# Kernel optimization log

Measured on AMD Instinct MI355X. Metric: run time of the kernel, lower is better.

The kernel has to match this reference:

```python
import jax, jax.numpy as jnp
import numpy as np

N_NODES = 50000


def gcn_layer(x, W, b, src, dst, n_nodes):
    # PyG GCNConv(normalize=True): add self-loops, deg^-1/2 sym norm,
    # x' = D^-1/2 (A+I) D^-1/2 (x W) + b, aggregation at dst (col).
    h = x @ W  # [N, out]
    ones = jnp.ones(src.shape[0], dtype=h.dtype)
    deg = jax.ops.segment_sum(ones, dst, num_segments=n_nodes) + 1.0  # +1 self-loop
    dinv = jax.lax.rsqrt(deg)  # [N]
    norm = dinv[src] * dinv[dst]  # per-edge coefficient
    msg = h[src] * norm[:, None]  # [E, out] gather
    agg = jax.ops.segment_sum(msg, dst, num_segments=n_nodes)  # scatter-add
    agg = agg + h * (dinv * dinv)[:, None]  # self-loop term (norm = dinv_i^2)
    return agg + b


def setup_inputs() -> dict:
    key = jax.random.key(0)
    k1, k2, k3, k4, k5 = jax.random.split(key, 5)
    x = jax.random.normal(k1, (N_NODES, 96), dtype=jnp.float32)
    edge_index = jax.random.randint(k2, (2, 800000), 0, N_NODES, dtype=jnp.int64)
    # Glorot-ish weights, zero bias (PyG default init style)
    W1 = jax.random.normal(k3, (96, 96), dtype=jnp.float32) * (1.0 / np.sqrt(96))
    b1 = jnp.zeros((96,), dtype=jnp.float32)
    W2 = jax.random.normal(k4, (96, 64), dtype=jnp.float32) * (1.0 / np.sqrt(96))
    b2 = jnp.zeros((64,), dtype=jnp.float32)
    return {"x": x, "edge_index": edge_index, "W1": W1, "b1": b1, "W2": W2, "b2": b2}


def reference(x, edge_index, W1, b1, W2, b2):
    src, dst = edge_index[0], edge_index[1]
    n = x.shape[0]
    h = gcn_layer(x, W1, b1, src, dst, n)
    out = gcn_layer(h, W2, b2, src, dst, n)
    return out
```

## Files before the change

### kernel.cpp

```cpp
#include <hip/hip_runtime.h>

#define N_NODES 50000
#define N_EDGES 800000
#define NBLKA 200
#define EPB (N_EDGES / NBLKA)
#define NBUCK 196
#define MSCAN (256 * NBLKA)
#define GEMMBLKS ((N_NODES + 63) / 64)

typedef unsigned int uint;
typedef unsigned short ushort;

__device__ __forceinline__ uint bf16pack(float a, float b) {
    uint ua = __float_as_uint(a); ua = (ua + 0x7FFFu + ((ua >> 16) & 1u)) >> 16;
    uint ub = __float_as_uint(b); ub = (ub + 0x7FFFu + ((ub >> 16) & 1u)) >> 16;
    return ua | (ub << 16);
}
#define BF_LO(U) __uint_as_float((U) << 16)
#define BF_HI(U) __uint_as_float((U) & 0xFFFF0000u)

__global__ void histA_kernel(const int* __restrict__ dst, int* __restrict__ hist) {
    __shared__ int h[256];
    h[threadIdx.x] = 0;
    __syncthreads();
    int base = blockIdx.x * EPB;
    for (int i = base + threadIdx.x; i < base + EPB; i += 256)
        atomicAdd(&h[dst[i] >> 8], 1);
    __syncthreads();
    hist[threadIdx.x * NBLKA + blockIdx.x] = h[threadIdx.x];
}

__global__ void scan1_kernel(const int* __restrict__ in, int* __restrict__ out,
                             int* __restrict__ bsum, int n) {
    __shared__ int s[256];
    int i = blockIdx.x * 256 + threadIdx.x;
    int v = (i < n) ? in[i] : 0;
    s[threadIdx.x] = v;
    __syncthreads();
    for (int d = 1; d < 256; d <<= 1) {
        int t = (threadIdx.x >= d) ? s[threadIdx.x - d] : 0;
        __syncthreads();
        s[threadIdx.x] += t;
        __syncthreads();
    }
    if (i < n) out[i] = s[threadIdx.x] - v;
    if (threadIdx.x == 255) bsum[blockIdx.x] = s[255];
}

__global__ void scan2_wfuse_kernel(int* __restrict__ bsum, int* __restrict__ boff, int nb,
                                   const float* __restrict__ W1, const float* __restrict__ W2,
                                   const float* __restrict__ b1, float* __restrict__ W12,
                                   float* __restrict__ bw) {
    if (blockIdx.x == 0) {
        __shared__ int s[256];
        int t = threadIdx.x;
        int v = (t < nb) ? bsum[t] : 0;
        s[t] = v;
        __syncthreads();
        for (int d = 1; d < 256; d <<= 1) {
            int x = (t >= d) ? s[t - d] : 0;
            __syncthreads();
            s[t] += x;
            __syncthreads();
        }
        if (t < nb) boff[t] = s[t] - v;
        if (t == nb - 1) boff[nb] = s[t];
    } else {
        int idx = (blockIdx.x - 1) * 256 + threadIdx.x;
        if (idx < 96 * 64) {
            int k = idx >> 6, nn = idx & 63;
            float s = 0.0f;
#pragma unroll
            for (int j = 0; j < 96; ++j) s = fmaf(W1[k * 96 + j], W2[j * 64 + nn], s);
            W12[idx] = s;
        } else if (idx < 96 * 64 + 64) {
            int nn = idx - 96 * 64;
            float s = 0.0f;
#pragma unroll
            for (int j = 0; j < 96; ++j) s = fmaf(b1[j], W2[j * 64 + nn], s);
            bw[nn] = s;
        }
    }
}

#define FMA4(ACC, SCL, WV)                                                     \
    ACC.x = fmaf(SCL, WV.x, ACC.x);                                            \
    ACC.y = fmaf(SCL, WV.y, ACC.y);                                            \
    ACC.z = fmaf(SCL, WV.z, ACC.z);                                            \
    ACC.w = fmaf(SCL, WV.w, ACC.w);

__global__ __launch_bounds__(256)
void scatter_gemm_kernel(const int* __restrict__ src, const int* __restrict__ dst,
                         const int* __restrict__ scanned, const int* __restrict__ boff,
                         int2* __restrict__ ebuf,
                         const float* __restrict__ A, const float* __restrict__ W,
                         ushort* __restrict__ y16, int M) {
    __shared__ float smem[96 * 64 + 64 * 100];
    int tid = threadIdx.x;

    if (blockIdx.x < NBLKA) {
        int* off = (int*)smem;
        int gi = tid * NBLKA + blockIdx.x;
        off[tid] = scanned[gi] + boff[gi >> 8];
        __syncthreads();
        int base = blockIdx.x * EPB;
        for (int i = base + tid; i < base + EPB; i += 256) {
            int s = src[i];
            int d = dst[i];
            int p = atomicAdd(&off[d >> 8], 1);
            ebuf[p] = make_int2(s, d);
        }
        return;
    }

    int bid = blockIdx.x - NBLKA;
    float* sW = smem;
    float* sA = smem + 96 * 64;
    {
        const float4* W4 = (const float4*)W;
        float4* sW4 = (float4*)sW;
        for (int i = tid; i < 96 * 16; i += 256) sW4[i] = W4[i];
    }
    long row0 = (long)bid * 64;
    {
        const float4* A4 = (const float4*)A;
        long base4 = row0 * 24;
        long lim = (long)M * 24 - 1;
        for (int f = tid; f < 64 * 24; f += 256) {
            long g = base4 + f;
            if (g > lim) g = lim;
            float4 v = A4[g];
            int r = f / 24, kc = f - r * 24;
            *(float4*)(sA + r * 100 + kc * 4) = v;
        }
    }
    __syncthreads();

    int tx = tid & 15;
    int ty = tid >> 4;
    float4 acc0 = {0, 0, 0, 0};
    float4 acc1 = {0, 0, 0, 0};
    float4 acc2 = {0, 0, 0, 0};
    float4 acc3 = {0, 0, 0, 0};
    const float* pa = sA + ty * 4 * 100;
    const float* pw = sW + tx * 4;

#pragma unroll 1
    for (int k = 0; k < 96; k += 4) {
        float4 a0 = *(const float4*)(pa + 0 * 100 + k);
        float4 a1 = *(const float4*)(pa + 1 * 100 + k);
        float4 a2 = *(const float4*)(pa + 2 * 100 + k);
        float4 a3 = *(const float4*)(pa + 3 * 100 + k);
        float4 w0 = *(const float4*)(pw + (k + 0) * 64);
        float4 w1 = *(const float4*)(pw + (k + 1) * 64);
        float4 w2 = *(const float4*)(pw + (k + 2) * 64);
        float4 w3 = *(const float4*)(pw + (k + 3) * 64);
        FMA4(acc0, a0.x, w0) FMA4(acc0, a0.y, w1) FMA4(acc0, a0.z, w2) FMA4(acc0, a0.w, w3)
        FMA4(acc1, a1.x, w0) FMA4(acc1, a1.y, w1) FMA4(acc1, a1.z, w2) FMA4(acc1, a1.w, w3)
        FMA4(acc2, a2.x, w0) FMA4(acc2, a2.y, w1) FMA4(acc2, a2.z, w2) FMA4(acc2, a2.w, w3)
        FMA4(acc3, a3.x, w0) FMA4(acc3, a3.y, w1) FMA4(acc3, a3.z, w2) FMA4(acc3, a3.w, w3)
    }

    long r0 = row0 + ty * 4;
    uint2 p0 = {bf16pack(acc0.x, acc0.y), bf16pack(acc0.z, acc0.w)};
    uint2 p1 = {bf16pack(acc1.x, acc1.y), bf16pack(acc1.z, acc1.w)};
    uint2 p2 = {bf16pack(acc2.x, acc2.y), bf16pack(acc2.z, acc2.w)};
    uint2 p3 = {bf16pack(acc3.x, acc3.y), bf16pack(acc3.z, acc3.w)};
    if (r0 + 0 < M) *(uint2*)(y16 + (r0 + 0) * 64 + tx * 4) = p0;
    if (r0 + 1 < M) *(uint2*)(y16 + (r0 + 1) * 64 + tx * 4) = p1;
    if (r0 + 2 < M) *(uint2*)(y16 + (r0 + 2) * 64 + tx * 4) = p2;
    if (r0 + 3 < M) *(uint2*)(y16 + (r0 + 3) * 64 + tx * 4) = p3;
}

__global__ void bucket_kernel(const int2* __restrict__ ebuf, const int* __restrict__ scanned,
                              const int* __restrict__ boff, int* __restrict__ rowstart,
                              float* __restrict__ dinv, int* __restrict__ esrc) {
    __shared__ int cnt[256];
    __shared__ int cur[256];
    __shared__ int s[256];
    int k = blockIdx.x;
    int tid = threadIdx.x;
    int i0 = k * NBLKA, i1 = (k + 1) * NBLKA;
    int base = scanned[i0] + boff[i0 >> 8];
    int end  = (k == NBUCK - 1) ? N_EDGES : (scanned[i1] + boff[i1 >> 8]);
    cnt[tid] = 0;
    __syncthreads();
    for (int i = base + tid; i < end; i += 256)
        atomicAdd(&cnt[ebuf[i].y & 255], 1);
    __syncthreads();
    int v = cnt[tid];
    s[tid] = v;
    __syncthreads();
    for (int d = 1; d < 256; d <<= 1) {
        int t = (tid >= d) ? s[tid - d] : 0;
        __syncthreads();
        s[tid] += t;
        __syncthreads();
    }
    int excl = s[tid] - v;
    int node = (k << 8) + tid;
    cur[tid] = base + excl;
    if (node < N_NODES) {
        rowstart[node] = base + excl;
        dinv[node] = rsqrtf((float)v + 1.0f);
    }
    if (k == 0 && tid == 0) rowstart[N_NODES] = N_EDGES;
    __syncthreads();
    for (int i = base + tid; i < end; i += 256) {
        int2 e = ebuf[i];
        int p = atomicAdd(&cur[e.y & 255], 1);
        esrc[p] = e.x;
    }
}

#define DECFMA(A0, A1, A2, A3, A4, A5, A6, A7, C, V)                           \
    A0 = fmaf(BF_LO(V.x), C, A0); A1 = fmaf(BF_HI(V.x), C, A1);                \
    A2 = fmaf(BF_LO(V.y), C, A2); A3 = fmaf(BF_HI(V.y), C, A3);                \
    A4 = fmaf(BF_LO(V.z), C, A4); A5 = fmaf(BF_HI(V.z), C, A5);                \
    A6 = fmaf(BF_LO(V.w), C, A6); A7 = fmaf(BF_HI(V.w), C, A7);

template <bool FINAL>
__global__ __launch_bounds__(256)
void agg_kernel(const ushort* __restrict__ yin, const int* __restrict__ rowstart,
                const int* __restrict__ esrc, const float* __restrict__ dinv,
                const float* __restrict__ bw, const float* __restrict__ b2,
                ushort* __restrict__ zout, float* __restrict__ fout, int n) {
    int wid = (blockIdx.x * blockDim.x + threadIdx.x) >> 6;
    int lane = threadIdx.x & 63;
    if (wid >= n) return;
    int rs = rowstart[wid];
    int re = rowstart[wid + 1];
    float di = dinv[wid];
    int sub = lane >> 3;
    int q = lane & 7;
    const uint4* yrow = (const uint4*)yin;
    float P0 = 0, P1 = 0, P2 = 0, P3 = 0, P4 = 0, P5 = 0, P6 = 0, P7 = 0;
    float Q0 = 0, Q1 = 0, Q2 = 0, Q3 = 0, Q4 = 0, Q5 = 0, Q6 = 0, Q7 = 0;
    float sd = 0.0f;

    for (int base = rs; base < re; base += 64) {
        int idx = base + lane;
        bool ok = idx < re;
        int sj = ok ? esrc[idx] : 0;
        float dj = ok ? dinv[sj] : 0.0f;
        sd += dj;
        int nn = re - base;
        if (nn > 64) nn = 64;
#pragma unroll 1
        for (int it = 0; it * 32 < nn; ++it) {
            int e0 = it * 32 + sub;
            int s0 = __shfl(sj, e0);      float c0 = __shfl(dj, e0);
            int s1 = __shfl(sj, e0 + 8);  float c1 = __shfl(dj, e0 + 8);
            int s2 = __shfl(sj, e0 + 16); float c2 = __shfl(dj, e0 + 16);
            int s3 = __shfl(sj, e0 + 24); float c3 = __shfl(dj, e0 + 24);
            uint4 v0 = yrow[(long)s0 * 8 + q];
            uint4 v1 = yrow[(long)s1 * 8 + q];
            uint4 v2 = yrow[(long)s2 * 8 + q];
            uint4 v3 = yrow[(long)s3 * 8 + q];
            DECFMA(P0, P1, P2, P3, P4, P5, P6, P7, c0, v0)
            DECFMA(Q0, Q1, Q2, Q3, Q4, Q5, Q6, Q7, c1, v1)
            DECFMA(P0, P1, P2, P3, P4, P5, P6, P7, c2, v2)
            DECFMA(Q0, Q1, Q2, Q3, Q4, Q5, Q6, Q7, c3, v3)
        }
    }

    float t0 = P0 + Q0, t1 = P1 + Q1, t2 = P2 + Q2, t3 = P3 + Q3;
    float t4 = P4 + Q4, t5 = P5 + Q5, t6 = P6 + Q6, t7 = P7 + Q7;
    t0 += __shfl_xor(t0, 8); t0 += __shfl_xor(t0, 16); t0 += __shfl_xor(t0, 32);
    t1 += __shfl_xor(t1, 8); t1 += __shfl_xor(t1, 16); t1 += __shfl_xor(t1, 32);
    t2 += __shfl_xor(t2, 8); t2 += __shfl_xor(t2, 16); t2 += __shfl_xor(t2, 32);
    t3 += __shfl_xor(t3, 8); t3 += __shfl_xor(t3, 16); t3 += __shfl_xor(t3, 32);
    t4 += __shfl_xor(t4, 8); t4 += __shfl_xor(t4, 16); t4 += __shfl_xor(t4, 32);
    t5 += __shfl_xor(t5, 8); t5 += __shfl_xor(t5, 16); t5 += __shfl_xor(t5, 32);
    t6 += __shfl_xor(t6, 8); t6 += __shfl_xor(t6, 16); t6 += __shfl_xor(t6, 32);
    t7 += __shfl_xor(t7, 8); t7 += __shfl_xor(t7, 16); t7 += __shfl_xor(t7, 32);

    uint4 sv = yrow[(long)wid * 8 + q];
    float dii = di * di;
    float o0 = fmaf(t0, di, BF_LO(sv.x) * dii);
    float o1 = fmaf(t1, di, BF_HI(sv.x) * dii);
    float o2 = fmaf(t2, di, BF_LO(sv.y) * dii);
    float o3 = fmaf(t3, di, BF_HI(sv.y) * dii);
    float o4 = fmaf(t4, di, BF_LO(sv.z) * dii);
    float o5 = fmaf(t5, di, BF_HI(sv.z) * dii);
    float o6 = fmaf(t6, di, BF_LO(sv.w) * dii);
    float o7 = fmaf(t7, di, BF_HI(sv.w) * dii);

    if (FINAL) {
#pragma unroll
        for (int m = 1; m < 64; m <<= 1) sd += __shfl_xor(sd, m);
        float si = di * (di + sd);
        int fo = q * 8;
        float4 bwa = *(const float4*)(bw + fo);
        float4 bwb = *(const float4*)(bw + fo + 4);
        float4 b2a = *(const float4*)(b2 + fo);
        float4 b2b = *(const float4*)(b2 + fo + 4);
        o0 = fmaf(si, bwa.x, o0) + b2a.x;
        o1 = fmaf(si, bwa.y, o1) + b2a.y;
        o2 = fmaf(si, bwa.z, o2) + b2a.z;
        o3 = fmaf(si, bwa.w, o3) + b2a.w;
        o4 = fmaf(si, bwb.x, o4) + b2b.x;
        o5 = fmaf(si, bwb.y, o5) + b2b.y;
        o6 = fmaf(si, bwb.z, o6) + b2b.z;
        o7 = fmaf(si, bwb.w, o7) + b2b.w;
        if (sub == 0) {
            float4 wa = {o0, o1, o2, o3};
            float4 wb = {o4, o5, o6, o7};
            *(float4*)(fout + (long)wid * 64 + q * 8) = wa;
            *(float4*)(fout + (long)wid * 64 + q * 8 + 4) = wb;
        }
    } else {
        if (sub == 0) {
            uint4 pk;
            pk.x = bf16pack(o0, o1);
            pk.y = bf16pack(o2, o3);
            pk.z = bf16pack(o4, o5);
            pk.w = bf16pack(o6, o7);
            *(uint4*)(zout + (long)wid * 64 + q * 8) = pk;
        }
    }
}

extern "C" void kernel_launch(void* const* d_in, const int* in_sizes, int n_in,
                              void* d_out, int out_size, void* d_ws, size_t ws_size,
                              hipStream_t stream) {
    const float* x  = (const float*)d_in[0];
    const int*   ei = (const int*)d_in[1];
    const float* W1 = (const float*)d_in[2];
    const float* b1 = (const float*)d_in[3];
    const float* W2 = (const float*)d_in[4];
    const float* b2 = (const float*)d_in[5];
    float* out = (float*)d_out;

    const int* src = ei;
    const int* dst = ei + N_EDGES;

    char* ws = (char*)d_ws;
    float*  dinv     = (float*) (ws + 0);
    int*    rowstart = (int*)   (ws + 204800);
    int*    hist     = (int*)   (ws + 409600);
    int*    scanned  = (int*)   (ws + 614400);
    int*    bsum     = (int*)   (ws + 823296);
    int*    boff     = (int*)   (ws + 824320);
    float*  W12      = (float*) (ws + 825344);
    float*  bw       = (float*) (ws + 849920);
    int*    esrc     = (int*)   (ws + 850432);
    ushort* y16      = (ushort*)(ws + 4050432);
    int2*   ebuf     = (int2*)  (ws + 10450432);
    ushort* z16      = (ushort*)(ws + 10450432);

    histA_kernel<<<NBLKA, 256, 0, stream>>>(dst, hist);
    scan1_kernel<<<MSCAN / 256, 256, 0, stream>>>(hist, scanned, bsum, MSCAN);
    scan2_wfuse_kernel<<<26, 256, 0, stream>>>(bsum, boff, MSCAN / 256,
                                               W1, W2, b1, W12, bw);
    scatter_gemm_kernel<<<NBLKA + GEMMBLKS, 256, 0, stream>>>(
        src, dst, scanned, boff, ebuf, x, W12, y16, N_NODES);

    bucket_kernel<<<NBUCK, 256, 0, stream>>>(ebuf, scanned, boff, rowstart, dinv, esrc);

    int aggBlocks = (N_NODES + 3) / 4;
    agg_kernel<false><<<aggBlocks, 256, 0, stream>>>(y16, rowstart, esrc, dinv,
                                                     bw, b2, z16, out, N_NODES);
    agg_kernel<true><<<aggBlocks, 256, 0, stream>>>(z16, rowstart, esrc, dinv,
                                                    bw, b2, z16, out, N_NODES);
}
```

Baseline: 98.97 us.

## Assign 16 lanes per node in aggregation and pack edge indices into 16 bits

The aggregation kernels now give each node a 16-lane group instead of a full 64-lane wavefront, so four nodes share a wavefront. With an average in-degree around 16, most lanes in the old layout sat idle. The reductions shrink to fit the smaller group. Separately, the sort buffer packs the source index and the low 8 bits of the destination into one 32-bit word, and the CSR source array becomes 16-bit, which cuts the bytes moved in the bucket and aggregation passes. This only works while the node count stays below 65536, and each lane now issues fewer independent gathers in flight.

```diff
diff --git a/kernel.cpp b/kernel.cpp
--- a/kernel.cpp
+++ b/kernel.cpp
@@ -92,7 +92,7 @@
 __global__ __launch_bounds__(256)
 void scatter_gemm_kernel(const int* __restrict__ src, const int* __restrict__ dst,
                          const int* __restrict__ scanned, const int* __restrict__ boff,
-                         int2* __restrict__ ebuf,
+                         uint* __restrict__ ebuf,
                          const float* __restrict__ A, const float* __restrict__ W,
                          ushort* __restrict__ y16, int M) {
     __shared__ float smem[96 * 64 + 64 * 100];
@@ -108,7 +108,7 @@
             int s = src[i];
             int d = dst[i];
             int p = atomicAdd(&off[d >> 8], 1);
-            ebuf[p] = make_int2(s, d);
+            ebuf[p] = (uint)s | ((uint)(d & 255) << 16);
         }
         return;
     }
@@ -172,9 +172,9 @@
     if (r0 + 3 < M) *(uint2*)(y16 + (r0 + 3) * 64 + tx * 4) = p3;
 }
 
-__global__ void bucket_kernel(const int2* __restrict__ ebuf, const int* __restrict__ scanned,
+__global__ void bucket_kernel(const uint* __restrict__ ebuf, const int* __restrict__ scanned,
                               const int* __restrict__ boff, int* __restrict__ rowstart,
-                              float* __restrict__ dinv, int* __restrict__ esrc) {
+                              float* __restrict__ dinv, ushort* __restrict__ esrc) {
     __shared__ int cnt[256];
     __shared__ int cur[256];
     __shared__ int s[256];
@@ -186,7 +186,7 @@
     cnt[tid] = 0;
     __syncthreads();
     for (int i = base + tid; i < end; i += 256)
-        atomicAdd(&cnt[ebuf[i].y & 255], 1);
+        atomicAdd(&cnt[(ebuf[i] >> 16) & 255], 1);
     __syncthreads();
     int v = cnt[tid];
     s[tid] = v;
@@ -207,9 +207,9 @@
     if (k == 0 && tid == 0) rowstart[N_NODES] = N_EDGES;
     __syncthreads();
     for (int i = base + tid; i < end; i += 256) {
-        int2 e = ebuf[i];
-        int p = atomicAdd(&cur[e.y & 255], 1);
-        esrc[p] = e.x;
+        uint e = ebuf[i];
+        int p = atomicAdd(&cur[(e >> 16) & 255], 1);
+        esrc[p] = (ushort)(e & 0xFFFFu);
     }
 }
 
@@ -222,60 +222,50 @@
 template <bool FINAL>
 __global__ __launch_bounds__(256)
 void agg_kernel(const ushort* __restrict__ yin, const int* __restrict__ rowstart,
-                const int* __restrict__ esrc, const float* __restrict__ dinv,
+                const ushort* __restrict__ esrc, const float* __restrict__ dinv,
                 const float* __restrict__ bw, const float* __restrict__ b2,
                 ushort* __restrict__ zout, float* __restrict__ fout, int n) {
-    int wid = (blockIdx.x * blockDim.x + threadIdx.x) >> 6;
-    int lane = threadIdx.x & 63;
-    if (wid >= n) return;
-    int rs = rowstart[wid];
-    int re = rowstart[wid + 1];
-    float di = dinv[wid];
-    int sub = lane >> 3;
-    int q = lane & 7;
+    int gid = (blockIdx.x * blockDim.x + threadIdx.x) >> 4;
+    int gl = threadIdx.x & 15;
+    if (gid >= n) return;
+    int rs = rowstart[gid];
+    int re = rowstart[gid + 1];
+    float di = dinv[gid];
+    int sub = gl >> 3;
+    int q = gl & 7;
+    int wbase = (threadIdx.x & 63) & 48;
     const uint4* yrow = (const uint4*)yin;
     float P0 = 0, P1 = 0, P2 = 0, P3 = 0, P4 = 0, P5 = 0, P6 = 0, P7 = 0;
-    float Q0 = 0, Q1 = 0, Q2 = 0, Q3 = 0, Q4 = 0, Q5 = 0, Q6 = 0, Q7 = 0;
     float sd = 0.0f;
 
-    for (int base = rs; base < re; base += 64) {
-        int idx = base + lane;
+    for (int base = rs; base < re; base += 16) {
+        int idx = base + gl;
         bool ok = idx < re;
-        int sj = ok ? esrc[idx] : 0;
+        int sj = ok ? (int)esrc[idx] : 0;
         float dj = ok ? dinv[sj] : 0.0f;
         sd += dj;
         int nn = re - base;
-        if (nn > 64) nn = 64;
-#pragma unroll 1
-        for (int it = 0; it * 32 < nn; ++it) {
-            int e0 = it * 32 + sub;
-            int s0 = __shfl(sj, e0);      float c0 = __shfl(dj, e0);
-            int s1 = __shfl(sj, e0 + 8);  float c1 = __shfl(dj, e0 + 8);
-            int s2 = __shfl(sj, e0 + 16); float c2 = __shfl(dj, e0 + 16);
-            int s3 = __shfl(sj, e0 + 24); float c3 = __shfl(dj, e0 + 24);
+        if (nn > 16) nn = 16;
+        for (int it = 0; it * 2 < nn; ++it) {
+            int e = it * 2 + sub;
+            int sl = wbase + e;
+            int s0 = __shfl(sj, sl);
+            float c0 = __shfl(dj, sl);
             uint4 v0 = yrow[(long)s0 * 8 + q];
-            uint4 v1 = yrow[(long)s1 * 8 + q];
-            uint4 v2 = yrow[(long)s2 * 8 + q];
-            uint4 v3 = yrow[(long)s3 * 8 + q];
             DECFMA(P0, P1, P2, P3, P4, P5, P6, P7, c0, v0)
-            DECFMA(Q0, Q1, Q2, Q3, Q4, Q5, Q6, Q7, c1, v1)
-            DECFMA(P0, P1, P2, P3, P4, P5, P6, P7, c2, v2)
-            DECFMA(Q0, Q1, Q2, Q3, Q4, Q5, Q6, Q7, c3, v3)
-        }
-    }
-
-    float t0 = P0 + Q0, t1 = P1 + Q1, t2 = P2 + Q2, t3 = P3 + Q3;
-    float t4 = P4 + Q4, t5 = P5 + Q5, t6 = P6 + Q6, t7 = P7 + Q7;
-    t0 += __shfl_xor(t0, 8); t0 += __shfl_xor(t0, 16); t0 += __shfl_xor(t0, 32);
-    t1 += __shfl_xor(t1, 8); t1 += __shfl_xor(t1, 16); t1 += __shfl_xor(t1, 32);
-    t2 += __shfl_xor(t2, 8); t2 += __shfl_xor(t2, 16); t2 += __shfl_xor(t2, 32);
-    t3 += __shfl_xor(t3, 8); t3 += __shfl_xor(t3, 16); t3 += __shfl_xor(t3, 32);
-    t4 += __shfl_xor(t4, 8); t4 += __shfl_xor(t4, 16); t4 += __shfl_xor(t4, 32);
-    t5 += __shfl_xor(t5, 8); t5 += __shfl_xor(t5, 16); t5 += __shfl_xor(t5, 32);
-    t6 += __shfl_xor(t6, 8); t6 += __shfl_xor(t6, 16); t6 += __shfl_xor(t6, 32);
-    t7 += __shfl_xor(t7, 8); t7 += __shfl_xor(t7, 16); t7 += __shfl_xor(t7, 32);
-
-    uint4 sv = yrow[(long)wid * 8 + q];
+        }
+    }
+
+    float t0 = P0 + __shfl_xor(P0, 8);
+    float t1 = P1 + __shfl_xor(P1, 8);
+    float t2 = P2 + __shfl_xor(P2, 8);
+    float t3 = P3 + __shfl_xor(P3, 8);
+    float t4 = P4 + __shfl_xor(P4, 8);
+    float t5 = P5 + __shfl_xor(P5, 8);
+    float t6 = P6 + __shfl_xor(P6, 8);
+    float t7 = P7 + __shfl_xor(P7, 8);
+
+    uint4 sv = yrow[(long)gid * 8 + q];
     float dii = di * di;
     float o0 = fmaf(t0, di, BF_LO(sv.x) * dii);
     float o1 = fmaf(t1, di, BF_HI(sv.x) * dii);
@@ -287,8 +277,8 @@
     float o7 = fmaf(t7, di, BF_HI(sv.w) * dii);
 
     if (FINAL) {
-#pragma unroll
-        for (int m = 1; m < 64; m <<= 1) sd += __shfl_xor(sd, m);
+        sd += __shfl_xor(sd, 1); sd += __shfl_xor(sd, 2);
+        sd += __shfl_xor(sd, 4); sd += __shfl_xor(sd, 8);
         float si = di * (di + sd);
         int fo = q * 8;
         float4 bwa = *(const float4*)(bw + fo);
@@ -306,8 +296,8 @@
         if (sub == 0) {
             float4 wa = {o0, o1, o2, o3};
             float4 wb = {o4, o5, o6, o7};
-            *(float4*)(fout + (long)wid * 64 + q * 8) = wa;
-            *(float4*)(fout + (long)wid * 64 + q * 8 + 4) = wb;
+            *(float4*)(fout + (long)gid * 64 + q * 8) = wa;
+            *(float4*)(fout + (long)gid * 64 + q * 8 + 4) = wb;
         }
     } else {
         if (sub == 0) {
@@ -316,7 +306,7 @@
             pk.y = bf16pack(o2, o3);
             pk.z = bf16pack(o4, o5);
             pk.w = bf16pack(o6, o7);
-            *(uint4*)(zout + (long)wid * 64 + q * 8) = pk;
+            *(uint4*)(zout + (long)gid * 64 + q * 8) = pk;
         }
     }
 }
@@ -344,10 +334,10 @@
     int*    boff     = (int*)   (ws + 824320);
     float*  W12      = (float*) (ws + 825344);
     float*  bw       = (float*) (ws + 849920);
-    int*    esrc     = (int*)   (ws + 850432);
-    ushort* y16      = (ushort*)(ws + 4050432);
-    int2*   ebuf     = (int2*)  (ws + 10450432);
-    ushort* z16      = (ushort*)(ws + 10450432);
+    ushort* esrc     = (ushort*)(ws + 850432);
+    ushort* y16      = (ushort*)(ws + 2450432);
+    uint*   ebuf     = (uint*)  (ws + 8850432);
+    ushort* z16      = (ushort*)(ws + 8850432);
 
     histA_kernel<<<NBLKA, 256, 0, stream>>>(dst, hist);
     scan1_kernel<<<MSCAN / 256, 256, 0, stream>>>(hist, scanned, bsum, MSCAN);
@@ -358,7 +348,7 @@
 
     bucket_kernel<<<NBUCK, 256, 0, stream>>>(ebuf, scanned, boff, rowstart, dinv, esrc);
 
-    int aggBlocks = (N_NODES + 3) / 4;
+    int aggBlocks = (N_NODES * 16 + 255) / 256;
     agg_kernel<false><<<aggBlocks, 256, 0, stream>>>(y16, rowstart, esrc, dinv,
                                                      bw, b2, z16, out, N_NODES);
     agg_kernel<true><<<aggBlocks, 256, 0, stream>>>(z16, rowstart, esrc, dinv,
```

Result: faster. 86.14 us (-13.0%).
